# Kernel tuning notes

Measured on AMD Instinct MI355X. Metric: run time of the kernel, lower is better.

## Reference

```python
import jax, jax.numpy as jnp
import numpy as np

IMAGE_W = 640
IMAGE_H = 640
MIN_SCORE = 0.05
NMS_THR = 0.5
MAX_DET = 100
B, A, C = 8, 76725, 80  # batch, total anchors over FPN levels (640x640, 9 anchors/loc), COCO classes


def setup_inputs() -> dict:
    key = jax.random.key(0)
    k1, k2, k3, k4, k5, k6 = jax.random.split(key, 6)
    # sigmoid-like class scores in [0,1]
    cls_heads = jax.random.uniform(k1, (B, A, C), dtype=jnp.float32)
    reg_heads = jax.random.normal(k2, (B, A, 4), dtype=jnp.float32) * 0.5
    # plausible anchors: centers in image, sizes in [16,256]
    cx = jax.random.uniform(k3, (B, A), dtype=jnp.float32) * IMAGE_W
    cy = jax.random.uniform(k4, (B, A), dtype=jnp.float32) * IMAGE_H
    w = jax.random.uniform(k5, (B, A), dtype=jnp.float32, minval=16.0, maxval=256.0)
    h = jax.random.uniform(k6, (B, A), dtype=jnp.float32, minval=16.0, maxval=256.0)
    batch_anchors = jnp.stack([cx - 0.5 * w, cy - 0.5 * h, cx + 0.5 * w, cy + 0.5 * h], axis=-1)
    return {"cls_heads": cls_heads, "reg_heads": reg_heads, "batch_anchors": batch_anchors}


def _decode(reg, anchors):
    # snap_tx_ty_tw_th_to_x1_y1_x2_y2: [A,4] deltas + [A,4] anchors -> int boxes
    wh = anchors[:, 2:] - anchors[:, :2]
    ctr = anchors[:, :2] + 0.5 * wh
    reg = reg * jnp.array([0.1, 0.1, 0.2, 0.2], dtype=reg.dtype)
    pwh = jnp.exp(reg[:, 2:]) * wh
    pctr = reg[:, :2] * wh + ctr
    boxes = jnp.concatenate([pctr - 0.5 * pwh, pctr + 0.5 * pwh], axis=1)
    boxes = boxes.astype(jnp.int32)  # torch .int() truncates toward zero, same as astype
    x1 = jnp.maximum(boxes[:, 0], 0)
    y1 = jnp.maximum(boxes[:, 1], 0)
    x2 = jnp.minimum(boxes[:, 2], IMAGE_W - 1)
    y2 = jnp.minimum(boxes[:, 3], IMAGE_H - 1)
    return jnp.stack([x1, y1, x2, y2], axis=1)


def _single_image(cls, reg, anchors):
    boxes = _decode(reg, anchors)              # [A,4] int32
    bf = boxes.astype(jnp.float32)
    scores = jnp.max(cls, axis=1)              # [A]
    classes = jnp.argmax(cls, axis=1)          # [A] int
    areas = (bf[:, 2] - bf[:, 0]) * (bf[:, 3] - bf[:, 1])
    work = jnp.where(scores > MIN_SCORE, scores, -jnp.inf)
    out_s = jnp.full((MAX_DET,), -1.0, jnp.float32)
    out_c = jnp.full((MAX_DET,), -1.0, jnp.float32)
    out_b = jnp.full((MAX_DET, 4), -1.0, jnp.float32)

    # Greedy global pick + per-class suppression == per-class NMS followed by
    # global descending sort + top MAX_DET (classes are independent under NMS).
    def body(i, carry):
        work, out_s, out_c, out_b = carry
        idx = jnp.argmax(work)
        s = work[idx]
        ok = jnp.isfinite(s)
        box = bf[idx]
        cls_i = classes[idx]
        xx1 = jnp.maximum(bf[:, 0], box[0])
        yy1 = jnp.maximum(bf[:, 1], box[1])
        xx2 = jnp.minimum(bf[:, 2], box[2])
        yy2 = jnp.minimum(bf[:, 3], box[3])
        inter = jnp.maximum(xx2 - xx1, 0.0) * jnp.maximum(yy2 - yy1, 0.0)
        union = areas + areas[idx] - inter
        iou = jnp.where(union > 0, inter / jnp.where(union > 0, union, 1.0), 0.0)
        suppress = (classes == cls_i) & (iou >= NMS_THR)  # keep mask was iou < thr
        work = jnp.where(ok & suppress, -jnp.inf, work)
        work = work.at[idx].set(-jnp.inf)
        out_s = out_s.at[i].set(jnp.where(ok, s, -1.0))
        out_c = out_c.at[i].set(jnp.where(ok, cls_i.astype(jnp.float32), -1.0))
        out_b = out_b.at[i].set(jnp.where(ok, box, -1.0))
        return (work, out_s, out_c, out_b)

    _, out_s, out_c, out_b = jax.lax.fori_loop(0, MAX_DET, body, (work, out_s, out_c, out_b))
    return out_s, out_c, out_b


def reference(cls_heads, reg_heads, batch_anchors):
    return jax.vmap(_single_image)(cls_heads, reg_heads, batch_anchors)
```

## Files before the change

### kernel.cpp

```cpp
#include <hip/hip_runtime.h>

#define NB 8
#define NA 76725
#define NC 80
#define MAXDET 100
#define CAP  1024
#define FTHR 0x3F7FF994u
#define TILE 64
#define NBLK 1199
#define GX   192
#define ST4  21

__device__ inline unsigned long long shfl_down_u64(unsigned long long v, int o) {
    unsigned lo = (unsigned)v, hi = (unsigned)(v >> 32);
    lo = __shfl_down(lo, o);
    hi = __shfl_down(hi, o);
    return ((unsigned long long)hi << 32) | lo;
}

__device__ inline unsigned long long shfl_xor_u64(unsigned long long v, int m) {
    unsigned lo = __shfl_xor((unsigned)v, m), hi = __shfl_xor((unsigned)(v >> 32), m);
    return ((unsigned long long)hi << 32) | lo;
}

__device__ inline bool iou_ge_half(float ax1, float ay1, float ax2, float ay2, float aar,
                                   float bx1, float by1, float bx2, float by2, float bar) {
    float xx1 = fmaxf(ax1, bx1), yy1 = fmaxf(ay1, by1);
    float xx2 = fminf(ax2, bx2), yy2 = fminf(ay2, by2);
    float inter = fmaxf(xx2 - xx1, 0.0f) * fmaxf(yy2 - yy1, 0.0f);
    float un = aar + bar - inter;
    float iou = (un > 0.0f) ? inter / un : 0.0f;
    return iou >= 0.5f;
}

__global__ __launch_bounds__(256) void k_map(const float* __restrict__ cls,
                                             const float* __restrict__ reg,
                                             const float* __restrict__ anc,
                                             unsigned long long* __restrict__ keys,
                                             unsigned long long* __restrict__ boxes,
                                             ulonglong2* __restrict__ cand,
                                             unsigned int* __restrict__ cnt_p,
                                             unsigned int* __restrict__ vws) {
    __shared__ float4 sc[TILE * ST4];
    __shared__ float4 s_rg[TILE];
    __shared__ float4 s_an[TILE];
    __shared__ unsigned s_v[4];
    const int b = blockIdx.y;
    const int tid = threadIdx.x;
    const int lane = tid & 63;
    const int wid = tid >> 6;
    const float4* cls4 = reinterpret_cast<const float4*>(cls);
    const float4* reg4 = reinterpret_cast<const float4*>(reg);
    const float4* anc4 = reinterpret_cast<const float4*>(anc);

    int tile = blockIdx.x;
    int n0 = tile * TILE;
    int ait = min(TILE, NA - n0);
    int nq = ait * 20;
    size_t base4 = ((size_t)b * NA + n0) * 20;

    float4 r0, r1, r2, r3, r4, ra;
#define LOADQ(K, RK) { int q = tid + (K)*256; if (q < nq) RK = cls4[base4 + q]; }
    LOADQ(0, r0) LOADQ(1, r1) LOADQ(2, r2) LOADQ(3, r3) LOADQ(4, r4)
    if (tid < 64) { if (tid < ait) ra = reg4[(size_t)b * NA + n0 + tid]; }
    else if (tid < 128) { if (tid - 64 < ait) ra = anc4[(size_t)b * NA + n0 + tid - 64]; }

    unsigned vacc = 0;
    for (;;) {
        __syncthreads();
#define STQ(K, RK) { int q = tid + (K)*256; if (q < nq) sc[(q / 20) * ST4 + (q % 20)] = RK; }
        STQ(0, r0) STQ(1, r1) STQ(2, r2) STQ(3, r3) STQ(4, r4)
        if (tid < 64) { if (tid < ait) s_rg[tid] = ra; }
        else if (tid < 128) { if (tid - 64 < ait) s_an[tid - 64] = ra; }
        __syncthreads();

        const int cn0 = n0, cait = ait;

        tile += GX;
        const bool more = tile < NBLK;
        if (more) {
            n0 = tile * TILE;
            ait = min(TILE, NA - n0);
            nq = ait * 20;
            base4 = ((size_t)b * NA + n0) * 20;
            LOADQ(0, r0) LOADQ(1, r1) LOADQ(2, r2) LOADQ(3, r3) LOADQ(4, r4)
            if (tid < 64) { if (tid < ait) ra = reg4[(size_t)b * NA + n0 + tid]; }
            else if (tid < 128) { if (tid - 64 < ait) ra = anc4[(size_t)b * NA + n0 + tid - 64]; }
        }

        const int a = tid >> 2, t = tid & 3;
        float best = -1.0f; int bc = 0;
#pragma unroll
        for (int j = 0; j < 5; ++j) {
            float4 v = sc[a * ST4 + t * 5 + j];
            if (v.x > best) { best = v.x; bc = t * 20 + 4 * j + 0; }
            if (v.y > best) { best = v.y; bc = t * 20 + 4 * j + 1; }
            if (v.z > best) { best = v.z; bc = t * 20 + 4 * j + 2; }
            if (v.w > best) { best = v.w; bc = t * 20 + 4 * j + 3; }
        }
        unsigned long long pk = ((unsigned long long)__float_as_uint(best) << 8)
                              | (unsigned)(255 - bc);
        pk = max(pk, shfl_xor_u64(pk, 1));
        pk = max(pk, shfl_xor_u64(pk, 2));

        bool valid = false, sel = false;
        unsigned long long key = 0ull, bp = 0ull;
        if (t == 0 && a < cait) {
            unsigned sbits = (unsigned)(pk >> 8);
            int cg = 255 - (int)(pk & 0xFFull);
            const int n_img = cn0 + a;
            const size_t n = (size_t)b * NA + n_img;
            float4 rg = s_rg[a];
            float4 an = s_an[a];

            float wx = __fsub_rn(an.z, an.x);
            float wy = __fsub_rn(an.w, an.y);
            float cx = __fadd_rn(an.x, __fmul_rn(0.5f, wx));
            float cy = __fadd_rn(an.y, __fmul_rn(0.5f, wy));
            float tx = __fmul_rn(rg.x, 0.1f), ty = __fmul_rn(rg.y, 0.1f);
            float tw = __fmul_rn(rg.z, 0.2f), th = __fmul_rn(rg.w, 0.2f);
            float pw = __fmul_rn(expf(tw), wx);
            float ph = __fmul_rn(expf(th), wy);
            float px = __fadd_rn(__fmul_rn(tx, wx), cx);
            float py = __fadd_rn(__fmul_rn(ty, wy), cy);
            int x1 = (int)__fsub_rn(px, __fmul_rn(0.5f, pw));
            int y1 = (int)__fsub_rn(py, __fmul_rn(0.5f, ph));
            int x2 = (int)__fadd_rn(px, __fmul_rn(0.5f, pw));
            int y2 = (int)__fadd_rn(py, __fmul_rn(0.5f, ph));
            x1 = max(x1, 0); y1 = max(y1, 0); x2 = min(x2, 639); y2 = min(y2, 639);

            bp = (unsigned long long)(unsigned short)(short)x1
               | ((unsigned long long)(unsigned short)(short)y1 << 16)
               | ((unsigned long long)(unsigned short)(short)x2 << 32)
               | ((unsigned long long)(unsigned short)(short)y2 << 48);
            float bestf = __uint_as_float(sbits);
            if (bestf > 0.05f) {
                unsigned inv = 0x1FFFFu - (unsigned)n_img;
                key = ((unsigned long long)sbits << 32) | ((unsigned long long)inv << 7)
                    | (unsigned)cg;
                valid = true;
                sel = sbits >= FTHR;
            }
            keys[n] = key;
            boxes[n] = bp;
        }

        unsigned long long bal = __ballot(valid);
        if (lane == 0) vacc += (unsigned)__popcll(bal);

        unsigned long long sbal = __ballot(sel);
        unsigned base = 0;
        if (lane == 0 && sbal) base = atomicAdd(&cnt_p[b * 32], (unsigned)__popcll(sbal));
        base = __shfl(base, 0);
        if (sel) {
            unsigned off = base + (unsigned)__popcll(sbal & ((1ull << lane) - 1ull));
            if (off < CAP) {
                ulonglong2 e; e.x = key; e.y = bp;
                cand[(size_t)b * CAP + off] = e;
            }
        }

        if (!more) break;
    }

    if (lane == 0) s_v[wid] = vacc;
    __syncthreads();
    if (tid == 0)
        vws[(size_t)b * GX + blockIdx.x] = s_v[0] + s_v[1] + s_v[2] + s_v[3];
}

__global__ __launch_bounds__(512) void k_nms(const ulonglong2* __restrict__ cand,
                                             const unsigned int* __restrict__ cnt_p,
                                             const unsigned int* __restrict__ vws,
                                             unsigned int* __restrict__ flag,
                                             float* __restrict__ out) {
    __shared__ unsigned long long sk[CAP];
    __shared__ unsigned long long sb[CAP];
    __shared__ int s_np;
    __shared__ unsigned s_ws[8];
    __shared__ unsigned s_vsum;
    const int b = blockIdx.x;
    unsigned total = cnt_p[b * 32];
    bool overflow = total > CAP;
    unsigned m = overflow ? CAP : total;

    unsigned local = 0;
    for (int j = threadIdx.x; j < GX; j += 512) local += vws[(size_t)b * GX + j];
    for (int o = 32; o > 0; o >>= 1) local += __shfl_down(local, o);
    if ((threadIdx.x & 63) == 0) s_ws[threadIdx.x >> 6] = local;

    for (int i = threadIdx.x; i < CAP; i += 512) {
        if (i < (int)m) { ulonglong2 e = cand[(size_t)b * CAP + i]; sk[i] = e.x; sb[i] = e.y; }
        else            { sk[i] = 0ull; sb[i] = 0ull; }
    }
    __syncthreads();
    if (threadIdx.x == 0) {
        unsigned s = 0;
        for (int w = 0; w < 8; ++w) s += s_ws[w];
        s_vsum = s;
    }

    for (int k = 2; k <= CAP; k <<= 1) {
        for (int j = k >> 1; j > 0; j >>= 1) {
            __syncthreads();
            int t = threadIdx.x;
            int i = ((t & ~(j - 1)) << 1) | (t & (j - 1));
            int l = i | j;
            unsigned long long ki = sk[i], kl = sk[l];
            bool desc = (i & k) == 0;
            if (desc ? (ki < kl) : (ki > kl)) {
                sk[i] = kl; sk[l] = ki;
                unsigned long long tmp = sb[i]; sb[i] = sb[l]; sb[l] = tmp;
            }
        }
    }
    __syncthreads();

    if (threadIdx.x < 64) {
        const int lane = threadIdx.x;
        float q0x1 = 0, q0y1 = 0, q0x2 = 0, q0y2 = 0, q0a = 0; int q0c = -1;
        float q1x1 = 0, q1y1 = 0, q1x2 = 0, q1y2 = 0, q1a = 0; int q1c = -1;
        int np = 0;
        unsigned long long nk = (m > 0) ? sk[0] : 0ull;
        unsigned long long nbx = (m > 0) ? sb[0] : 0ull;
        for (int jj = 0; jj < (int)m && np < MAXDET; ++jj) {
            unsigned long long key = nk;
            unsigned long long bx = nbx;
            if (jj + 1 < (int)m) { nk = sk[jj + 1]; nbx = sb[jj + 1]; }
            if (!key) break;
            int ci = (int)(key & 0x7Full);
            float x1 = (float)(short)(bx & 0xFFFF);
            float y1 = (float)(short)((bx >> 16) & 0xFFFF);
            float x2 = (float)(short)((bx >> 32) & 0xFFFF);
            float y2 = (float)(short)((bx >> 48) & 0xFFFF);
            float ar = (x2 - x1) * (y2 - y1);
            bool sup = false;
            if (lane < np && q0c == ci)
                sup = iou_ge_half(q0x1, q0y1, q0x2, q0y2, q0a, x1, y1, x2, y2, ar);
            if (64 + lane < np && q1c == ci)
                sup = sup || iou_ge_half(q1x1, q1y1, q1x2, q1y2, q1a, x1, y1, x2, y2, ar);
            if (__ballot(sup) != 0ull) continue;
            int s = np;
            if (s < 64) {
                if (lane == s) {
                    q0x1 = x1; q0y1 = y1; q0x2 = x2; q0y2 = y2; q0a = ar; q0c = ci;
                    out[b * MAXDET + s] = __uint_as_float((unsigned)(key >> 32));
                    out[NB * MAXDET + b * MAXDET + s] = (float)ci;
                    float* ob = out + 2 * NB * MAXDET + (size_t)(b * MAXDET + s) * 4;
                    ob[0] = x1; ob[1] = y1; ob[2] = x2; ob[3] = y2;
                }
            } else {
                if (lane == s - 64) {
                    q1x1 = x1; q1y1 = y1; q1x2 = x2; q1y2 = y2; q1a = ar; q1c = ci;
                    out[b * MAXDET + s] = __uint_as_float((unsigned)(key >> 32));
                    out[NB * MAXDET + b * MAXDET + s] = (float)ci;
                    float* ob = out + 2 * NB * MAXDET + (size_t)(b * MAXDET + s) * 4;
                    ob[0] = x1; ob[1] = y1; ob[2] = x2; ob[3] = y2;
                }
            }
            ++np;
        }
        if (lane == 0) s_np = np;
    }
    __syncthreads();
    int np = s_np;
    bool fb = overflow || (np < MAXDET && s_vsum > m);
    if (threadIdx.x == 0) flag[b] = fb ? 1u : 0u;
    if (!fb) {
        for (int i = np + (int)threadIdx.x; i < MAXDET; i += 512) {
            out[b * MAXDET + i] = -1.0f;
            out[NB * MAXDET + b * MAXDET + i] = -1.0f;
            float* ob = out + 2 * NB * MAXDET + (size_t)(b * MAXDET + i) * 4;
            ob[0] = -1.0f; ob[1] = -1.0f; ob[2] = -1.0f; ob[3] = -1.0f;
        }
    }
}

__global__ __launch_bounds__(1024) void k_fallback(unsigned long long* __restrict__ keys,
                                                   const unsigned long long* __restrict__ boxes,
                                                   const unsigned int* __restrict__ flag,
                                                   float* __restrict__ out) {
    const int b = blockIdx.x;
    if (!flag[b]) return;
    __shared__ unsigned long long wm[16];
    __shared__ unsigned long long gbest;
    unsigned long long* kb = keys + (size_t)b * NA;
    const unsigned long long* bb = boxes + (size_t)b * NA;

    for (int it = 0; it < MAXDET; ++it) {
        unsigned long long best = 0ull;
        for (int i = threadIdx.x; i < NA; i += 1024) {
            unsigned long long k = kb[i];
            if (k > best) best = k;
        }
        for (int o = 32; o > 0; o >>= 1) {
            unsigned long long v = shfl_down_u64(best, o);
            if (v > best) best = v;
        }
        if ((threadIdx.x & 63) == 0) wm[threadIdx.x >> 6] = best;
        __syncthreads();
        if (threadIdx.x == 0) {
            unsigned long long g = wm[0];
            for (int w = 1; w < 16; ++w) if (wm[w] > g) g = wm[w];
            gbest = g;
        }
        __syncthreads();
        best = gbest;
        if (best == 0ull) {
            for (int s = it + (int)threadIdx.x; s < MAXDET; s += 1024) {
                out[b * MAXDET + s] = -1.0f;
                out[NB * MAXDET + b * MAXDET + s] = -1.0f;
                float* ob = out + 2 * NB * MAXDET + (size_t)(b * MAXDET + s) * 4;
                ob[0] = -1.0f; ob[1] = -1.0f; ob[2] = -1.0f; ob[3] = -1.0f;
            }
            break;
        }
        int ci = (int)(best & 0x7Full);
        int a = 0x1FFFF - (int)((best >> 7) & 0x1FFFFull);
        unsigned long long bx = bb[a];
        float x1 = (float)(short)(bx & 0xFFFF);
        float y1 = (float)(short)((bx >> 16) & 0xFFFF);
        float x2 = (float)(short)((bx >> 32) & 0xFFFF);
        float y2 = (float)(short)((bx >> 48) & 0xFFFF);
        float ar = (x2 - x1) * (y2 - y1);
        if (threadIdx.x == 0) {
            out[b * MAXDET + it] = __uint_as_float((unsigned)(best >> 32));
            out[NB * MAXDET + b * MAXDET + it] = (float)ci;
            float* ob = out + 2 * NB * MAXDET + (size_t)(b * MAXDET + it) * 4;
            ob[0] = x1; ob[1] = y1; ob[2] = x2; ob[3] = y2;
        }
        for (int i = threadIdx.x; i < NA; i += 1024) {
            unsigned long long kk = kb[i];
            if (!kk) continue;
            if (kk == best) { kb[i] = 0ull; continue; }
            if ((int)(kk & 0x7Full) != ci) continue;
            unsigned long long ob2 = bb[i];
            float u1 = (float)(short)(ob2 & 0xFFFF);
            float v1 = (float)(short)((ob2 >> 16) & 0xFFFF);
            float u2 = (float)(short)((ob2 >> 32) & 0xFFFF);
            float v2 = (float)(short)((ob2 >> 48) & 0xFFFF);
            float oar = (u2 - u1) * (v2 - v1);
            if (iou_ge_half(x1, y1, x2, y2, ar, u1, v1, u2, v2, oar)) kb[i] = 0ull;
        }
        __syncthreads();
    }
}

extern "C" void kernel_launch(void* const* d_in, const int* in_sizes, int n_in,
                              void* d_out, int out_size, void* d_ws, size_t ws_size,
                              hipStream_t stream) {
    const float* cls = (const float*)d_in[0];
    const float* reg = (const float*)d_in[1];
    const float* anc = (const float*)d_in[2];
    float* out = (float*)d_out;

    const size_t SZ_KEYS = (size_t)NB * NA * 8;
    unsigned long long* keys  = (unsigned long long*)d_ws;
    unsigned long long* boxes = (unsigned long long*)((char*)d_ws + SZ_KEYS);
    ulonglong2* cand = (ulonglong2*)((char*)d_ws + 2 * SZ_KEYS);
    unsigned* cnt_p = (unsigned*)((char*)d_ws + 2 * SZ_KEYS + (size_t)NB * CAP * 16);
    unsigned* vws   = cnt_p + NB * 32;
    unsigned* flag  = vws + (size_t)NB * GX;

    hipMemsetAsync(cnt_p, 0, NB * 32 * 4, stream);

    dim3 gmap(GX, NB);
    k_map<<<gmap, 256, 0, stream>>>(cls, reg, anc, keys, boxes, cand, cnt_p, vws);
    k_nms<<<NB, 512, 0, stream>>>(cand, cnt_p, vws, flag, out);
    k_fallback<<<NB, 1024, 0, stream>>>(keys, boxes, flag, out);
}
```

Before: 333.0 us.

## Replace global candidate atomic counter with per-block slots and prefix-sum compaction

Each map block now appends its high-score candidates into its own fixed-size slot segment, counting with a shared-memory atomic instead of a per-image global atomic. The NMS kernel prefix-sums the per-block counts to compact the segments into shared memory before sorting. This also removes the hipMemsetAsync that zeroed the global counter. The costs are a larger candidate workspace and a fallback to the slow path whenever any block holds more than SLOT candidates.

```diff
diff --git a/kernel.cpp b/kernel.cpp
--- a/kernel.cpp
+++ b/kernel.cpp
@@ -9,6 +9,7 @@
 #define TILE 64
 #define NBLK 1199
 #define GX   192
+#define SLOT 32
 #define ST4  21
 
 __device__ inline unsigned long long shfl_down_u64(unsigned long long v, int o) {
@@ -39,12 +40,13 @@
                                              unsigned long long* __restrict__ keys,
                                              unsigned long long* __restrict__ boxes,
                                              ulonglong2* __restrict__ cand,
-                                             unsigned int* __restrict__ cnt_p,
+                                             unsigned int* __restrict__ scnt,
                                              unsigned int* __restrict__ vws) {
     __shared__ float4 sc[TILE * ST4];
     __shared__ float4 s_rg[TILE];
     __shared__ float4 s_an[TILE];
     __shared__ unsigned s_v[4];
+    __shared__ unsigned s_cnt;
     const int b = blockIdx.y;
     const int tid = threadIdx.x;
     const int lane = tid & 63;
@@ -52,6 +54,9 @@
     const float4* cls4 = reinterpret_cast<const float4*>(cls);
     const float4* reg4 = reinterpret_cast<const float4*>(reg);
     const float4* anc4 = reinterpret_cast<const float4*>(anc);
+    ulonglong2* seg = cand + ((size_t)b * GX + blockIdx.x) * SLOT;
+
+    if (tid == 0) s_cnt = 0;
 
     int tile = blockIdx.x;
     int n0 = tile * TILE;
@@ -150,13 +155,13 @@
 
         unsigned long long sbal = __ballot(sel);
         unsigned base = 0;
-        if (lane == 0 && sbal) base = atomicAdd(&cnt_p[b * 32], (unsigned)__popcll(sbal));
+        if (lane == 0 && sbal) base = atomicAdd(&s_cnt, (unsigned)__popcll(sbal));
         base = __shfl(base, 0);
         if (sel) {
             unsigned off = base + (unsigned)__popcll(sbal & ((1ull << lane) - 1ull));
-            if (off < CAP) {
+            if (off < SLOT) {
                 ulonglong2 e; e.x = key; e.y = bp;
-                cand[(size_t)b * CAP + off] = e;
+                seg[off] = e;
             }
         }
 
@@ -165,45 +170,68 @@
 
     if (lane == 0) s_v[wid] = vacc;
     __syncthreads();
-    if (tid == 0)
+    if (tid == 0) {
         vws[(size_t)b * GX + blockIdx.x] = s_v[0] + s_v[1] + s_v[2] + s_v[3];
+        scnt[(size_t)b * GX + blockIdx.x] = s_cnt;
+    }
 }
 
 __global__ __launch_bounds__(512) void k_nms(const ulonglong2* __restrict__ cand,
-                                             const unsigned int* __restrict__ cnt_p,
+                                             const unsigned int* __restrict__ scnt,
                                              const unsigned int* __restrict__ vws,
                                              unsigned int* __restrict__ flag,
                                              float* __restrict__ out) {
     __shared__ unsigned long long sk[CAP];
     __shared__ unsigned long long sb[CAP];
     __shared__ int s_np;
-    __shared__ unsigned s_ws[8];
+    __shared__ unsigned s_w[8];
+    __shared__ unsigned s_vw[8];
+    __shared__ unsigned s_total;
     __shared__ unsigned s_vsum;
+    __shared__ unsigned s_ovf;
     const int b = blockIdx.x;
-    unsigned total = cnt_p[b * 32];
-    bool overflow = total > CAP;
-    unsigned m = overflow ? CAP : total;
-
-    unsigned local = 0;
-    for (int j = threadIdx.x; j < GX; j += 512) local += vws[(size_t)b * GX + j];
-    for (int o = 32; o > 0; o >>= 1) local += __shfl_down(local, o);
-    if ((threadIdx.x & 63) == 0) s_ws[threadIdx.x >> 6] = local;
-
-    for (int i = threadIdx.x; i < CAP; i += 512) {
-        if (i < (int)m) { ulonglong2 e = cand[(size_t)b * CAP + i]; sk[i] = e.x; sb[i] = e.y; }
-        else            { sk[i] = 0ull; sb[i] = 0ull; }
-    }
-    __syncthreads();
-    if (threadIdx.x == 0) {
-        unsigned s = 0;
-        for (int w = 0; w < 8; ++w) s += s_ws[w];
-        s_vsum = s;
-    }
+    const int tid = threadIdx.x, lane = tid & 63, wid = tid >> 6;
+    if (tid == 0) s_ovf = 0;
+    __syncthreads();
+
+    unsigned c = 0, v = 0;
+    if (tid < GX) { c = scnt[(size_t)b * GX + tid]; v = vws[(size_t)b * GX + tid]; }
+    if (c > SLOT) { s_ovf = 1; c = SLOT; }
+
+    unsigned x = c;
+    for (int o = 1; o < 64; o <<= 1) { unsigned y = __shfl_up(x, o); if (lane >= o) x += y; }
+    unsigned vv = v;
+    for (int o = 32; o > 0; o >>= 1) vv += __shfl_down(vv, o);
+    if (lane == 63) s_w[wid] = x;
+    if (lane == 0) s_vw[wid] = vv;
+    __syncthreads();
+    if (tid == 0) {
+        unsigned r = 0;
+        for (int w = 0; w < 8; ++w) { unsigned t2 = s_w[w]; s_w[w] = r; r += t2; }
+        s_total = r;
+        unsigned vs = 0;
+        for (int w = 0; w < 8; ++w) vs += s_vw[w];
+        s_vsum = vs;
+    }
+    for (int i = tid; i < CAP; i += 512) { sk[i] = 0ull; sb[i] = 0ull; }
+    __syncthreads();
+    unsigned excl = x - c + s_w[wid];
+    unsigned total = s_total;
+    bool overflow = (s_ovf != 0) || (total > CAP);
+    unsigned m = (total > CAP) ? CAP : total;
+
+    if (tid < GX) {
+        const ulonglong2* seg = cand + ((size_t)b * GX + tid) * SLOT;
+        for (unsigned k2 = 0; k2 < c; ++k2) {
+            unsigned idx = excl + k2;
+            if (idx < CAP) { ulonglong2 e = seg[k2]; sk[idx] = e.x; sb[idx] = e.y; }
+        }
+    }
+    __syncthreads();
 
     for (int k = 2; k <= CAP; k <<= 1) {
         for (int j = k >> 1; j > 0; j >>= 1) {
-            __syncthreads();
-            int t = threadIdx.x;
+            int t = tid;
             int i = ((t & ~(j - 1)) << 1) | (t & (j - 1));
             int l = i | j;
             unsigned long long ki = sk[i], kl = sk[l];
@@ -212,12 +240,11 @@
                 sk[i] = kl; sk[l] = ki;
                 unsigned long long tmp = sb[i]; sb[i] = sb[l]; sb[l] = tmp;
             }
-        }
-    }
-    __syncthreads();
-
-    if (threadIdx.x < 64) {
-        const int lane = threadIdx.x;
+            __syncthreads();
+        }
+    }
+
+    if (tid < 64) {
         float q0x1 = 0, q0y1 = 0, q0x2 = 0, q0y2 = 0, q0a = 0; int q0c = -1;
         float q1x1 = 0, q1y1 = 0, q1x2 = 0, q1y2 = 0, q1a = 0; int q1c = -1;
         int np = 0;
@@ -265,9 +292,9 @@
     __syncthreads();
     int np = s_np;
     bool fb = overflow || (np < MAXDET && s_vsum > m);
-    if (threadIdx.x == 0) flag[b] = fb ? 1u : 0u;
+    if (tid == 0) flag[b] = fb ? 1u : 0u;
     if (!fb) {
-        for (int i = np + (int)threadIdx.x; i < MAXDET; i += 512) {
+        for (int i = np + tid; i < MAXDET; i += 512) {
             out[b * MAXDET + i] = -1.0f;
             out[NB * MAXDET + b * MAXDET + i] = -1.0f;
             float* ob = out + 2 * NB * MAXDET + (size_t)(b * MAXDET + i) * 4;
@@ -358,14 +385,12 @@
     unsigned long long* keys  = (unsigned long long*)d_ws;
     unsigned long long* boxes = (unsigned long long*)((char*)d_ws + SZ_KEYS);
     ulonglong2* cand = (ulonglong2*)((char*)d_ws + 2 * SZ_KEYS);
-    unsigned* cnt_p = (unsigned*)((char*)d_ws + 2 * SZ_KEYS + (size_t)NB * CAP * 16);
-    unsigned* vws   = cnt_p + NB * 32;
-    unsigned* flag  = vws + (size_t)NB * GX;
-
-    hipMemsetAsync(cnt_p, 0, NB * 32 * 4, stream);
+    unsigned* scnt = (unsigned*)((char*)d_ws + 2 * SZ_KEYS + (size_t)NB * GX * SLOT * 16);
+    unsigned* vws  = scnt + (size_t)NB * GX;
+    unsigned* flag = vws + (size_t)NB * GX;
 
     dim3 gmap(GX, NB);
-    k_map<<<gmap, 256, 0, stream>>>(cls, reg, anc, keys, boxes, cand, cnt_p, vws);
-    k_nms<<<NB, 512, 0, stream>>>(cand, cnt_p, vws, flag, out);
+    k_map<<<gmap, 256, 0, stream>>>(cls, reg, anc, keys, boxes, cand, scnt, vws);
+    k_nms<<<NB, 512, 0, stream>>>(cand, scnt, vws, flag, out);
     k_fallback<<<NB, 1024, 0, stream>>>(keys, boxes, flag, out);
 }
```

After: 336.3 us. Within noise of the previous version (+1.0%).
